# Kernel tuning notes

Measured on AMD Instinct MI355X. Metric: run time of the kernel, lower is better.

The kernel has to match this reference:

```python
import jax, jax.numpy as jnp
import numpy as np

N = 100000       # num_nodes
E = 1600000      # num edges
C = 1000         # num_communities
NE = 128         # n_embedding
NID = 64         # n_id_embedding
NH = 128         # n_hidden


def setup_inputs() -> dict:
    key = jax.random.key(0)
    ks = jax.random.split(key, 24)
    s = 0.05  # small init scale for weights
    inp = {
        "x": jax.random.normal(ks[0], (N, 19), dtype=jnp.float32),
        "edge_index": jax.random.randint(ks[1], (2, E), 0, N, dtype=jnp.int64),
        "community": jax.random.randint(ks[2], (N,), 0, C, dtype=jnp.int64),
        "id_embeddings": jax.random.normal(ks[3], (N, NID), dtype=jnp.float32),
        "W_emb1": jax.random.normal(ks[4], (7, NE), dtype=jnp.float32) * s,
        "b_emb1": jnp.zeros((NE,), jnp.float32),
        "W_emb2": jax.random.normal(ks[5], (12, NE), dtype=jnp.float32) * s,
        "b_emb2": jnp.zeros((NE,), jnp.float32),
        "W_emb3": jax.random.normal(ks[6], (2 * NE + NID, 2 * NE + NID), dtype=jnp.float32) * s,
        "b_emb3": jnp.zeros((2 * NE + NID,), jnp.float32),
        "W_conv1": jax.random.normal(ks[7], (2 * NE + NID, NH), dtype=jnp.float32) * s,
        "b_conv1": jnp.zeros((NH,), jnp.float32),
        "W_conv2": jax.random.normal(ks[8], (NH, NH), dtype=jnp.float32) * s,
        "b_conv2": jnp.zeros((NH,), jnp.float32),
        "W_lin1": jax.random.normal(ks[9], (2 * NH, NH), dtype=jnp.float32) * s,
        "b_lin1": jnp.zeros((NH,), jnp.float32),
        "W_lin2": jax.random.normal(ks[10], (NH, 1), dtype=jnp.float32) * s,
        "b_lin2": jnp.zeros((1,), jnp.float32),
    }
    return inp


def _gcn_conv(h, W, b, src, dst, deg_inv_sqrt):
    # PyG GCNConv: D^{-1/2}(A+I)D^{-1/2} (h W) + b, self-loops included.
    hw = h @ W                                   # [N, out]
    norm = deg_inv_sqrt[src] * deg_inv_sqrt[dst]  # [E]
    msg = hw[src] * norm[:, None]                # [E, out] gather
    agg = jax.ops.segment_sum(msg, dst, num_segments=N)
    agg = agg + hw * (deg_inv_sqrt ** 2)[:, None]  # self-loop term (norm = 1/deg)
    return agg + b


def _community_pool(h, community):
    # scatter_mean over community ids, then cat([mean, mean], dim=1)
    sums = jax.ops.segment_sum(h, community, num_segments=C)
    cnt = jax.ops.segment_sum(jnp.ones((h.shape[0],), h.dtype), community, num_segments=C)
    mean = sums / jnp.maximum(cnt, 1.0)[:, None]
    return jnp.concatenate([mean, mean], axis=1)


def reference(x, edge_index, community, id_embeddings,
              W_emb1, b_emb1, W_emb2, b_emb2, W_emb3, b_emb3,
              W_conv1, b_conv1, W_conv2, b_conv2,
              W_lin1, b_lin1, W_lin2, b_lin2):
    src, dst = edge_index[0], edge_index[1]
    # degree (with self-loops) on dst, as in PyG gcn_norm
    deg = jax.ops.segment_sum(jnp.ones((E,), jnp.float32), dst, num_segments=N) + 1.0
    deg_inv_sqrt = deg ** -0.5

    x1 = jax.nn.relu(x[:, :7] @ W_emb1 + b_emb1)
    x2 = jax.nn.relu(x[:, 7:] @ W_emb2 + b_emb2)
    h = jnp.concatenate([x1, x2, id_embeddings], axis=1)   # [N, 320]
    h = jax.nn.relu(h @ W_emb3 + b_emb3)

    h = jax.nn.relu(_gcn_conv(h, W_conv1, b_conv1, src, dst, deg_inv_sqrt))
    p1 = _community_pool(h, community)                      # [C, 2*NH]
    h = jax.nn.relu(_gcn_conv(h, W_conv2, b_conv2, src, dst, deg_inv_sqrt))
    p2 = _community_pool(h, community)                      # [C, 2*NH]

    z = p1 + p2
    z = jax.nn.relu(z @ W_lin1 + b_lin1)
    # dropout is identity in eval mode (training=False)
    out = (z @ W_lin2 + b_lin2).squeeze(-1)                 # [C]
    return out
```

## Files before the change

### kernel.cpp

```cpp
#include <hip/hip_runtime.h>
#include <hip/hip_bf16.h>
#include <cstddef>

#define NN 100000
#define EE 1600000
#define CC 1000
#define NBK ((NN + 255) / 256)
#define EPB 4096

#define FP8_SCALE 32.0f
#define FP8_INV   0.03125f

using short8 = __attribute__((ext_vector_type(8))) short;
using f32x4  = __attribute__((ext_vector_type(4))) float;
using f32x2  = __attribute__((ext_vector_type(2))) float;

__device__ __forceinline__ float bf2f(unsigned int u) {
    union { unsigned int i; float f; } x; x.i = u << 16; return x.f;
}
__device__ __forceinline__ unsigned short f2bf(float f) {
    __hip_bfloat16 h = __float2bfloat16(f);
    return *reinterpret_cast<unsigned short*>(&h);
}
__device__ __forceinline__ unsigned int pack2(float lo, float hi) {
    return ((unsigned int)f2bf(hi) << 16) | f2bf(lo);
}
__device__ __forceinline__ unsigned char f2fp8(float v) {
    unsigned int p = __builtin_amdgcn_cvt_pk_fp8_f32(v, v, 0, false);
    return (unsigned char)(p & 0xffu);
}
__device__ __forceinline__ f32x2 fp8x2f(unsigned int u16) {
    return __builtin_amdgcn_cvt_pk_f32_fp8(u16, false);
}

__global__ void k_init(int* __restrict__ bucketCnt, int* __restrict__ bucketFill,
                       int* __restrict__ commcnt) {
    int i = blockIdx.x * 256 + threadIdx.x;
    if (i < NBK) { bucketCnt[i] = 0; bucketFill[i] = 0; }
    if (i < CC) commcnt[i] = 0;
}

__global__ __launch_bounds__(256) void k_bhist(const int* __restrict__ dst,
                                               int* __restrict__ bucketCnt) {
    __shared__ int hist[NBK];
    int t = threadIdx.x;
    for (int i = t; i < NBK; i += 256) hist[i] = 0;
    __syncthreads();
    int base = blockIdx.x * EPB;
    for (int i = t; i < EPB; i += 256) {
        int e = base + i;
        if (e < EE) atomicAdd(&hist[dst[e] >> 8], 1);
    }
    __syncthreads();
    for (int i = t; i < NBK; i += 256)
        if (hist[i]) atomicAdd(&bucketCnt[i], hist[i]);
}

__global__ void k_bscan(const int* __restrict__ bucketCnt, int* __restrict__ bucketBase) {
    __shared__ int sd[512];
    int t = threadIdx.x;
    int v = (t < NBK) ? bucketCnt[t] : 0;
    sd[t] = v;
    __syncthreads();
    for (int off = 1; off < 512; off <<= 1) {
        int x = (t >= off) ? sd[t - off] : 0;
        __syncthreads();
        sd[t] += x;
        __syncthreads();
    }
    if (t < NBK) bucketBase[t] = sd[t] - v;
    if (t == 0) bucketBase[NBK] = EE;
}

__global__ __launch_bounds__(256) void k_bucketize(
    const int* __restrict__ src, const int* __restrict__ dst,
    const int* __restrict__ bucketBase, int* __restrict__ bucketFill,
    int2* __restrict__ bkt) {
    __shared__ int hist[NBK];
    __shared__ int runPos[NBK];
    int t = threadIdx.x;
    for (int i = t; i < NBK; i += 256) hist[i] = 0;
    __syncthreads();
    int base = blockIdx.x * EPB;
    for (int i = t; i < EPB; i += 256) {
        int e = base + i;
        if (e < EE) atomicAdd(&hist[dst[e] >> 8], 1);
    }
    __syncthreads();
    for (int i = t; i < NBK; i += 256)
        runPos[i] = hist[i] ? (bucketBase[i] + atomicAdd(&bucketFill[i], hist[i])) : 0;
    __syncthreads();
    for (int i = t; i < EPB; i += 256) {
        int e = base + i;
        if (e < EE) {
            int d = dst[e];
            int pos = atomicAdd(&runPos[d >> 8], 1);
            bkt[pos] = make_int2(src[e], d);
        }
    }
}

__global__ __launch_bounds__(256) void k_csr(
    const int2* __restrict__ bkt, const int* __restrict__ bucketBase,
    const int* __restrict__ comm, int* __restrict__ commcnt,
    int* __restrict__ rowofs, float* __restrict__ dis, int* __restrict__ csr) {
    __shared__ int cnt[256], sd[256], cnt2[256];
    int b = blockIdx.x, t = threadIdx.x;
    int base = bucketBase[b], end = bucketBase[b + 1];
    int nodeBase = b << 8;
    cnt[t] = 0; cnt2[t] = 0;
    __syncthreads();
    for (int i = base + t; i < end; i += 256)
        atomicAdd(&cnt[bkt[i].y - nodeBase], 1);
    __syncthreads();
    int v = cnt[t];
    sd[t] = v;
    __syncthreads();
    for (int off = 1; off < 256; off <<= 1) {
        int x = (t >= off) ? sd[t - off] : 0;
        __syncthreads();
        sd[t] += x;
        __syncthreads();
    }
    int ofs = sd[t] - v;
    sd[t] = ofs;
    int node = nodeBase + t;
    if (node < NN) {
        rowofs[node] = base + ofs;
        dis[node] = rsqrtf((float)v + 1.0f);
        atomicAdd(&commcnt[comm[node]], 1);
    }
    if (b == NBK - 1 && t == 0) rowofs[NN] = EE;
    __syncthreads();
    for (int i = base + t; i < end; i += 256) {
        int2 ed = bkt[i];
        int ld = ed.y - nodeBase;
        int p = atomicAdd(&cnt2[ld], 1);
        csr[base + sd[ld] + p] = ed.x;
    }
}

__global__ void k_scanc(int* __restrict__ commcnt, int* __restrict__ commofs) {
    __shared__ int sd[1024];
    int t = threadIdx.x;
    int v = (t < CC) ? commcnt[t] : 0;
    sd[t] = v;
    __syncthreads();
    for (int off = 1; off < 1024; off <<= 1) {
        int x = (t >= off) ? sd[t - off] : 0;
        __syncthreads();
        sd[t] += x;
        __syncthreads();
    }
    if (t < CC) {
        commofs[t] = sd[t] - v;
        commcnt[t] = 0;
    }
    if (t == CC - 1) commofs[CC] = sd[t];
}

__global__ void k_fillc(const int* __restrict__ comm, const int* __restrict__ commofs,
                        int* __restrict__ commcnt, int* __restrict__ members) {
    int i = blockIdx.x * 256 + threadIdx.x;
    if (i >= NN) return;
    int c = comm[i];
    int pos = commofs[c] + atomicAdd(&commcnt[c], 1);
    members[pos] = i;
}

__global__ void k_wconv(const float* __restrict__ W3, unsigned short* __restrict__ W3t,
                        const float* __restrict__ Wc1, unsigned short* __restrict__ Wc1t,
                        const float* __restrict__ Wc2, unsigned short* __restrict__ Wc2t) {
    int y = blockIdx.y;
    int k = blockIdx.x * 256 + threadIdx.x;
    if (y < 320) {
        if (k < 328) W3t[(size_t)y * 328 + k] = (k < 320) ? f2bf(W3[(size_t)k * 320 + y]) : 0;
    } else if (y < 448) {
        int n = y - 320;
        if (k < 328) Wc1t[(size_t)n * 328 + k] = (k < 320) ? f2bf(Wc1[(size_t)k * 128 + n]) : 0;
    } else {
        int n = y - 448;
        if (k < 136) Wc2t[(size_t)n * 136 + k] = (k < 128) ? f2bf(Wc2[(size_t)k * 128 + n]) : 0;
    }
}

__global__ __launch_bounds__(256) void k_embed(
    const float* __restrict__ x, const float* __restrict__ id_emb,
    const float* __restrict__ W1, const float* __restrict__ b1,
    const float* __restrict__ W2, const float* __restrict__ b2,
    unsigned short* __restrict__ h0) {
    __shared__ float W1s[7][128];
    __shared__ float W2s[12][128];
    __shared__ float b1s[128], b2s[128];
    __shared__ float xs[64][20];
    int t = threadIdx.x;
    int base = blockIdx.x * 64;
    for (int i = t; i < 7 * 128; i += 256) ((float*)W1s)[i] = W1[i];
    for (int i = t; i < 12 * 128; i += 256) ((float*)W2s)[i] = W2[i];
    if (t < 128) { b1s[t] = b1[t]; b2s[t] = b2[t]; }
    for (int i = t; i < 64 * 19; i += 256) {
        int r = i / 19, cc = i % 19;
        int node = base + r;
        xs[r][cc] = (node < NN) ? x[(size_t)node * 19 + cc] : 0.f;
    }
    __syncthreads();
    int ln = t >> 6, lane = t & 63;
    int c2 = lane * 2;
    for (int nn = ln; nn < 64; nn += 4) {
        int node = base + nn;
        if (node >= NN) break;
        unsigned int* orow = (unsigned int*)(h0 + (size_t)node * 320);
        float a0 = b1s[c2], a1 = b1s[c2 + 1];
        #pragma unroll
        for (int k = 0; k < 7; ++k) {
            float xv = xs[nn][k];
            float2 w = *(const float2*)&W1s[k][c2];
            a0 += xv * w.x; a1 += xv * w.y;
        }
        orow[lane] = pack2(fmaxf(a0, 0.f), fmaxf(a1, 0.f));
        a0 = b2s[c2]; a1 = b2s[c2 + 1];
        #pragma unroll
        for (int k = 0; k < 12; ++k) {
            float xv = xs[nn][7 + k];
            float2 w = *(const float2*)&W2s[k][c2];
            a0 += xv * w.x; a1 += xv * w.y;
        }
        orow[64 + lane] = pack2(fmaxf(a0, 0.f), fmaxf(a1, 0.f));
        if (lane < 32) {
            float2 iv = *(const float2*)(id_emb + (size_t)node * 64 + c2);
            orow[128 + lane] = pack2(iv.x, iv.y);
        }
    }
}

template <int K, int N, int RELU, int OUT8>
__global__ __launch_bounds__(256) void k_bgemm(
    const unsigned short* __restrict__ A, const unsigned short* __restrict__ Bt,
    const float* __restrict__ bias, void* __restrict__ Cv, int M) {
    constexpr int NT = (N + 127) / 128;
    __shared__ __align__(16) short sbuf[2][10240];
    int t = threadIdx.x;
    int bid = blockIdx.x;
    if constexpr (NT > 1) {
        int nwg = gridDim.x;
        int q = nwg >> 3, r = nwg & 7;
        int xcd = bid & 7, idx = bid >> 3;
        bid = (xcd < r ? xcd * (q + 1) : r * (q + 1) + (xcd - r) * q) + idx;
    }
    int ct = bid % NT, rblk = bid / NT;
    int rowBase = rblk * 128, colBase = ct * 128;
    int wid = t >> 6, lane = t & 63;
    int wm = wid >> 1, wn = wid & 1;
    int fr = lane & 15, g = lane >> 4;
    int rr = t >> 2;
    int qq = (t & 3) * 8;
    f32x4 acc[4][4] = {};
    short8 z = {};
    short8 pA0, pA1, pB0, pB1;
    int grA0 = rowBase + rr, grA1 = grA0 + 64;
    int gcB0 = colBase + rr, gcB1 = gcB0 + 64;
    pA0 = (grA0 < M) ? *(const short8*)(A + (size_t)grA0 * K + qq) : z;
    pA1 = (grA1 < M) ? *(const short8*)(A + (size_t)grA1 * K + qq) : z;
    pB0 = (gcB0 < N) ? *(const short8*)(Bt + (size_t)gcB0 * (K + 8) + qq) : z;
    pB1 = (gcB1 < N) ? *(const short8*)(Bt + (size_t)gcB1 * (K + 8) + qq) : z;
    {
        short* As = sbuf[0];
        short* Bs = sbuf[0] + 128 * 40;
        *(short8*)&As[rr * 40 + qq]        = pA0;
        *(short8*)&As[(rr + 64) * 40 + qq] = pA1;
        *(short8*)&Bs[rr * 40 + qq]        = pB0;
        *(short8*)&Bs[(rr + 64) * 40 + qq] = pB1;
    }
    __syncthreads();
    int cur = 0;
    for (int kb = 0; kb < K; kb += 32) {
        bool more = (kb + 32 < K);
        if (more) {
            int kn = kb + 32;
            pA0 = (grA0 < M) ? *(const short8*)(A + (size_t)grA0 * K + kn + qq) : z;
            pA1 = (grA1 < M) ? *(const short8*)(A + (size_t)grA1 * K + kn + qq) : z;
            pB0 = (gcB0 < N) ? *(const short8*)(Bt + (size_t)gcB0 * (K + 8) + kn + qq) : z;
            pB1 = (gcB1 < N) ? *(const short8*)(Bt + (size_t)gcB1 * (K + 8) + kn + qq) : z;
        }
        const short* As = sbuf[cur];
        const short* Bs = sbuf[cur] + 128 * 40;
        short8 bfr[4];
        #pragma unroll
        for (int nf = 0; nf < 4; ++nf)
            bfr[nf] = *(const short8*)&Bs[(wn * 64 + nf * 16 + fr) * 40 + g * 8];
        #pragma unroll
        for (int mf = 0; mf < 4; ++mf) {
            short8 a = *(const short8*)&As[(wm * 64 + mf * 16 + fr) * 40 + g * 8];
            #pragma unroll
            for (int nf = 0; nf < 4; ++nf)
                acc[mf][nf] = __builtin_amdgcn_mfma_f32_16x16x32_bf16(a, bfr[nf], acc[mf][nf], 0, 0, 0);
        }
        if (more) {
            short* Asn = sbuf[cur ^ 1];
            short* Bsn = sbuf[cur ^ 1] + 128 * 40;
            *(short8*)&Asn[rr * 40 + qq]        = pA0;
            *(short8*)&Asn[(rr + 64) * 40 + qq] = pA1;
            *(short8*)&Bsn[rr * 40 + qq]        = pB0;
            *(short8*)&Bsn[(rr + 64) * 40 + qq] = pB1;
        }
        __syncthreads();
        cur ^= 1;
    }
    if (!OUT8) {
        unsigned short* sb = (unsigned short*)sbuf[0];
        #pragma unroll
        for (int cc = 0; cc < 2; ++cc) {
            int cbase = colBase + cc * 64;
            if (cbase < N) {
                if (cc) __syncthreads();
                if (wn == cc) {
                    #pragma unroll
                    for (int nf = 0; nf < 4; ++nf) {
                        int colL = nf * 16 + fr;
                        float bv = RELU ? bias[cbase + colL] : 0.f;
                        #pragma unroll
                        for (int mf = 0; mf < 4; ++mf) {
                            #pragma unroll
                            for (int r = 0; r < 4; ++r) {
                                int row = wm * 64 + mf * 16 + g * 4 + r;
                                float v = acc[mf][nf][r];
                                if (RELU) v = fmaxf(v + bv, 0.f);
                                sb[row * 72 + colL] = f2bf(v);
                            }
                        }
                    }
                }
                __syncthreads();
                #pragma unroll
                for (int i = 0; i < 4; ++i) {
                    int off8 = t + 256 * i;
                    int row = off8 >> 3;
                    int col = (off8 & 7) * 8;
                    int grow = rowBase + row;
                    if (grow < M)
                        *(short8*)((unsigned short*)Cv + (size_t)grow * N + cbase + col) =
                            *(const short8*)&sb[row * 72 + col];
                }
            }
        }
    } else {
        unsigned char* sb8 = (unsigned char*)sbuf[0];
        #pragma unroll
        for (int nf = 0; nf < 4; ++nf) {
            int colL = wn * 64 + nf * 16 + fr;
            #pragma unroll
            for (int mf = 0; mf < 4; ++mf) {
                #pragma unroll
                for (int r = 0; r < 4; ++r) {
                    int row = wm * 64 + mf * 16 + g * 4 + r;
                    sb8[row * 128 + colL] = f2fp8(acc[mf][nf][r] * FP8_SCALE);
                }
            }
        }
        __syncthreads();
        #pragma unroll
        for (int i = 0; i < 4; ++i) {
            int off16 = t + 256 * i;
            int row = off16 >> 3;
            int col = (off16 & 7) * 16;
            int grow = rowBase + row;
            if (grow < M)
                *(int4*)((unsigned char*)Cv + (size_t)grow * N + col) =
                    *(const int4*)&sb8[row * 128 + col];
        }
    }
}

__global__ __launch_bounds__(256) void k_gather(
    const int* __restrict__ rowofs, const int* __restrict__ csr,
    const float* __restrict__ dis, const unsigned char* __restrict__ hw8,
    const float* __restrict__ bias, unsigned short* __restrict__ hout) {
    int wid = blockIdx.x * 4 + (threadIdx.x >> 6);
    wid = __builtin_amdgcn_readfirstlane(wid);
    int lane = threadIdx.x & 63;
    if (wid >= NN) return;
    int ro = rowofs[wid], re = rowofs[wid + 1];
    int c = lane * 2;
    float dsd = dis[wid];
    unsigned int hv = *(const unsigned short*)(hw8 + (size_t)wid * 128 + c);
    f32x2 hf = fp8x2f(hv);
    float a0 = hf.x * dsd;
    float a1 = hf.y * dsd;
    int e = ro;
    for (; e + 16 <= re; e += 16) {
        int s[16]; float n[16]; unsigned int v[16];
        #pragma unroll
        for (int j = 0; j < 16; ++j) s[j] = csr[e + j];
        #pragma unroll
        for (int j = 0; j < 16; ++j) n[j] = dis[s[j]];
        #pragma unroll
        for (int j = 0; j < 16; ++j)
            v[j] = *(const unsigned short*)(hw8 + (size_t)s[j] * 128 + c);
        #pragma unroll
        for (int j = 0; j < 16; ++j) {
            f32x2 f = fp8x2f(v[j]);
            a0 += f.x * n[j];
            a1 += f.y * n[j];
        }
    }
    for (; e + 4 <= re; e += 4) {
        int s[4]; float n[4]; unsigned int v[4];
        #pragma unroll
        for (int j = 0; j < 4; ++j) s[j] = csr[e + j];
        #pragma unroll
        for (int j = 0; j < 4; ++j) n[j] = dis[s[j]];
        #pragma unroll
        for (int j = 0; j < 4; ++j)
            v[j] = *(const unsigned short*)(hw8 + (size_t)s[j] * 128 + c);
        #pragma unroll
        for (int j = 0; j < 4; ++j) {
            f32x2 f = fp8x2f(v[j]);
            a0 += f.x * n[j];
            a1 += f.y * n[j];
        }
    }
    for (; e < re; ++e) {
        int s0 = csr[e];
        float n0 = dis[s0];
        unsigned int v0 = *(const unsigned short*)(hw8 + (size_t)s0 * 128 + c);
        f32x2 f = fp8x2f(v0);
        a0 += f.x * n0;
        a1 += f.y * n0;
    }
    a0 = fmaxf(a0 * dsd * FP8_INV + bias[c], 0.f);
    a1 = fmaxf(a1 * dsd * FP8_INV + bias[c + 1], 0.f);
    *(unsigned int*)(hout + (size_t)wid * 128 + c) = pack2(a0, a1);
}

__global__ __launch_bounds__(128) void k_final(
    const unsigned short* __restrict__ h2, const unsigned short* __restrict__ h3,
    const int* __restrict__ commofs, const int* __restrict__ members,
    const float* __restrict__ Wl1, const float* __restrict__ bl1,
    const float* __restrict__ Wl2, const float* __restrict__ bl2,
    float* __restrict__ out) {
    __shared__ float zh[128];
    __shared__ float partial[2];
    int c = blockIdx.x, t = threadIdx.x;
    int ro = commofs[c], re = commofs[c + 1];
    float acc = 0.f;
    int e = ro;
    for (; e + 4 <= re; e += 4) {
        int m0 = members[e], m1 = members[e + 1];
        int m2 = members[e + 2], m3 = members[e + 3];
        acc += bf2f(h2[(size_t)m0 * 128 + t]) + bf2f(h3[(size_t)m0 * 128 + t]);
        acc += bf2f(h2[(size_t)m1 * 128 + t]) + bf2f(h3[(size_t)m1 * 128 + t]);
        acc += bf2f(h2[(size_t)m2 * 128 + t]) + bf2f(h3[(size_t)m2 * 128 + t]);
        acc += bf2f(h2[(size_t)m3 * 128 + t]) + bf2f(h3[(size_t)m3 * 128 + t]);
    }
    for (; e < re; ++e) {
        int m = members[e];
        acc += bf2f(h2[(size_t)m * 128 + t]) + bf2f(h3[(size_t)m * 128 + t]);
    }
    float invc = 1.0f / fmaxf((float)(re - ro), 1.0f);
    zh[t] = acc * invc;
    __syncthreads();
    float a = bl1[t];
    for (int k = 0; k < 128; ++k)
        a += zh[k] * (Wl1[(size_t)k * 128 + t] + Wl1[(size_t)(k + 128) * 128 + t]);
    float zv = fmaxf(a, 0.f);
    float p = zv * Wl2[t];
    #pragma unroll
    for (int off = 32; off > 0; off >>= 1) p += __shfl_down(p, off, 64);
    if ((t & 63) == 0) partial[t >> 6] = p;
    __syncthreads();
    if (t == 0) out[c] = partial[0] + partial[1] + bl2[0];
}

extern "C" void kernel_launch(void* const* d_in, const int* in_sizes, int n_in,
                              void* d_out, int out_size, void* d_ws, size_t ws_size,
                              hipStream_t stream) {
    const float* x       = (const float*)d_in[0];
    const int*   edge    = (const int*)d_in[1];
    const int*   comm    = (const int*)d_in[2];
    const float* id_emb  = (const float*)d_in[3];
    const float* W1      = (const float*)d_in[4];
    const float* b1      = (const float*)d_in[5];
    const float* W2      = (const float*)d_in[6];
    const float* b2      = (const float*)d_in[7];
    const float* W3      = (const float*)d_in[8];
    const float* b3      = (const float*)d_in[9];
    const float* Wc1     = (const float*)d_in[10];
    const float* bc1     = (const float*)d_in[11];
    const float* Wc2     = (const float*)d_in[12];
    const float* bc2     = (const float*)d_in[13];
    const float* Wl1     = (const float*)d_in[14];
    const float* bl1     = (const float*)d_in[15];
    const float* Wl2     = (const float*)d_in[16];
    const float* bl2     = (const float*)d_in[17];
    float* out = (float*)d_out;
    float* ws  = (float*)d_ws;

    const int* srcIdx = edge;
    const int* dstIdx = edge + EE;

    size_t o = 0;
    auto alloc = [&](size_t nfloats) {
        float* p = ws + o; o += (nfloats + 3) & ~(size_t)3; return p;
    };
    float* dis      = alloc(NN);
    int* rowofs     = (int*)alloc(NN + 8);
    int* bucketCnt  = (int*)alloc(NBK + 8);
    int* bucketBase = (int*)alloc(NBK + 8);
    int* bucketFill = (int*)alloc(NBK + 8);
    int* commcnt    = (int*)alloc(1024);
    int* commofs    = (int*)alloc(1024 + 8);
    int* members    = (int*)alloc(NN);
    int2* bkt       = (int2*)alloc((size_t)EE * 2);
    int* csr        = (int*)alloc(EE);
    unsigned short* W3t  = (unsigned short*)alloc(320 * 328 / 2);
    unsigned short* Wc1t = (unsigned short*)alloc(128 * 328 / 2);
    unsigned short* Wc2t = (unsigned short*)alloc(128 * 136 / 2);
    unsigned short* h0   = (unsigned short*)alloc((size_t)NN * 320 / 2);
    unsigned short* h1   = (unsigned short*)alloc((size_t)NN * 320 / 2);
    unsigned char*  hw8  = (unsigned char*)alloc((size_t)NN * 128 / 4);
    unsigned short* h2   = (unsigned short*)alloc((size_t)NN * 128 / 2);
    unsigned short* h3   = (unsigned short*)alloc((size_t)NN * 128 / 2);

    k_init<<<4, 256, 0, stream>>>(bucketCnt, bucketFill, commcnt);
    k_bhist<<<NBK, 256, 0, stream>>>(dstIdx, bucketCnt);
    k_bscan<<<1, 512, 0, stream>>>(bucketCnt, bucketBase);
    k_bucketize<<<NBK, 256, 0, stream>>>(srcIdx, dstIdx, bucketBase, bucketFill, bkt);
    k_csr<<<NBK, 256, 0, stream>>>(bkt, bucketBase, comm, commcnt, rowofs, dis, csr);
    k_scanc<<<1, 1024, 0, stream>>>(commcnt, commofs);
    k_fillc<<<NBK, 256, 0, stream>>>(comm, commofs, commcnt, members);

    k_wconv<<<dim3(2, 576), 256, 0, stream>>>(W3, W3t, Wc1, Wc1t, Wc2, Wc2t);

    k_embed<<<(NN + 63) / 64, 256, 0, stream>>>(x, id_emb, W1, b1, W2, b2, h0);

    int rb = (NN + 127) / 128;
    k_bgemm<320, 320, 1, 0><<<rb * 3, 256, 0, stream>>>(h0, W3t, b3, h1, NN);
    k_bgemm<320, 128, 0, 1><<<rb, 256, 0, stream>>>(h1, Wc1t, nullptr, hw8, NN);
    k_gather<<<(NN + 3) / 4, 256, 0, stream>>>(rowofs, csr, dis, hw8, bc1, h2);
    k_bgemm<128, 128, 0, 1><<<rb, 256, 0, stream>>>(h2, Wc2t, nullptr, hw8, NN);
    k_gather<<<(NN + 3) / 4, 256, 0, stream>>>(rowofs, csr, dis, hw8, bc2, h3);

    k_final<<<CC, 128, 0, stream>>>(h2, h3, commofs, members, Wl1, bl1, Wl2, bl2, out);
}
```

Measured before the change: 380.8 us.

## Fuse embedding GEMM and conv1 GEMM into one kernel keeping intermediate in LDS

A new kernel computes relu(h0·W3+b3) for a 64-row tile, keeps the result in shared memory, and immediately multiplies it by Wc1 to produce the FP8 hw8 output. This drops the global write and reread of the 320-wide bf16 intermediate and one kernel launch. The unused bf16 output path and the XCD block remapping are removed from the generic GEMM. The trade-off is large LDS use, which lowers occupancy, plus single-buffered weight tiles reloaded per block with no prefetch overlap.

```diff
diff --git a/kernel.cpp b/kernel.cpp
--- a/kernel.cpp
+++ b/kernel.cpp
@@ -233,6 +233,104 @@
     }
 }
 
+__global__ __launch_bounds__(256) void k_fuse(
+    const unsigned short* __restrict__ h0, const unsigned short* __restrict__ W3t,
+    const float* __restrict__ b3, const unsigned short* __restrict__ Wc1t,
+    unsigned char* __restrict__ hw8, int M) {
+    __shared__ __align__(16) short h0s[64][328];
+    __shared__ __align__(16) short Bs[320][40];
+    int t = threadIdx.x;
+    int rowBase = blockIdx.x * 64;
+    int w = t >> 6, lane = t & 63;
+    int fr = lane & 15, g = lane >> 4;
+    for (int c = t; c < 64 * 40; c += 256) {
+        int r = c / 40, part = c % 40;
+        int grow = rowBase + r;
+        short8 v = {};
+        if (grow < M) v = *(const short8*)(h0 + (size_t)grow * 320 + part * 8);
+        *(short8*)&h0s[r][part * 8] = v;
+    }
+    f32x4 acc1[4][5] = {};
+    for (int kb = 0; kb < 320; kb += 32) {
+        __syncthreads();
+        for (int c = t; c < 320 * 4; c += 256) {
+            int r = c >> 2, q = c & 3;
+            *(short8*)&Bs[r][q * 8] = *(const short8*)(W3t + (size_t)r * 328 + kb + q * 8);
+        }
+        __syncthreads();
+        short8 a[4], b[5];
+        #pragma unroll
+        for (int rf = 0; rf < 4; ++rf)
+            a[rf] = *(const short8*)&h0s[rf * 16 + fr][kb + g * 8];
+        #pragma unroll
+        for (int cf = 0; cf < 5; ++cf)
+            b[cf] = *(const short8*)&Bs[w * 80 + cf * 16 + fr][g * 8];
+        #pragma unroll
+        for (int rf = 0; rf < 4; ++rf)
+            #pragma unroll
+            for (int cf = 0; cf < 5; ++cf)
+                acc1[rf][cf] = __builtin_amdgcn_mfma_f32_16x16x32_bf16(a[rf], b[cf], acc1[rf][cf], 0, 0, 0);
+    }
+    __syncthreads();
+    #pragma unroll
+    for (int cf = 0; cf < 5; ++cf) {
+        int col = w * 80 + cf * 16 + fr;
+        float bv = b3[col];
+        #pragma unroll
+        for (int rf = 0; rf < 4; ++rf) {
+            #pragma unroll
+            for (int r = 0; r < 4; ++r) {
+                int row = rf * 16 + g * 4 + r;
+                h0s[row][col] = (short)f2bf(fmaxf(acc1[rf][cf][r] + bv, 0.f));
+            }
+        }
+    }
+    f32x4 acc2[4][2] = {};
+    for (int kb = 0; kb < 320; kb += 32) {
+        __syncthreads();
+        for (int c = t; c < 128 * 4; c += 256) {
+            int r = c >> 2, q = c & 3;
+            *(short8*)&Bs[r][q * 8] = *(const short8*)(Wc1t + (size_t)r * 328 + kb + q * 8);
+        }
+        __syncthreads();
+        short8 a[4], b[2];
+        #pragma unroll
+        for (int rf = 0; rf < 4; ++rf)
+            a[rf] = *(const short8*)&h0s[rf * 16 + fr][kb + g * 8];
+        #pragma unroll
+        for (int cf = 0; cf < 2; ++cf)
+            b[cf] = *(const short8*)&Bs[w * 32 + cf * 16 + fr][g * 8];
+        #pragma unroll
+        for (int rf = 0; rf < 4; ++rf)
+            #pragma unroll
+            for (int cf = 0; cf < 2; ++cf)
+                acc2[rf][cf] = __builtin_amdgcn_mfma_f32_16x16x32_bf16(a[rf], b[cf], acc2[rf][cf], 0, 0, 0);
+    }
+    unsigned char* sb8 = (unsigned char*)Bs;
+    __syncthreads();
+    #pragma unroll
+    for (int cf = 0; cf < 2; ++cf) {
+        int colL = w * 32 + cf * 16 + fr;
+        #pragma unroll
+        for (int rf = 0; rf < 4; ++rf) {
+            #pragma unroll
+            for (int r = 0; r < 4; ++r) {
+                int row = rf * 16 + g * 4 + r;
+                sb8[row * 128 + colL] = f2fp8(acc2[rf][cf][r] * FP8_SCALE);
+            }
+        }
+    }
+    __syncthreads();
+    #pragma unroll
+    for (int i = 0; i < 2; ++i) {
+        int c16 = t + 256 * i;
+        int row = c16 >> 3, col = (c16 & 7) * 16;
+        int grow = rowBase + row;
+        if (grow < M)
+            *(int4*)(hw8 + (size_t)grow * 128 + col) = *(const int4*)&sb8[row * 128 + col];
+    }
+}
+
 template <int K, int N, int RELU, int OUT8>
 __global__ __launch_bounds__(256) void k_bgemm(
     const unsigned short* __restrict__ A, const unsigned short* __restrict__ Bt,
@@ -241,12 +339,6 @@
     __shared__ __align__(16) short sbuf[2][10240];
     int t = threadIdx.x;
     int bid = blockIdx.x;
-    if constexpr (NT > 1) {
-        int nwg = gridDim.x;
-        int q = nwg >> 3, r = nwg & 7;
-        int xcd = bid & 7, idx = bid >> 3;
-        bid = (xcd < r ? xcd * (q + 1) : r * (q + 1) + (xcd - r) * q) + idx;
-    }
     int ct = bid % NT, rblk = bid / NT;
     int rowBase = rblk * 128, colBase = ct * 128;
     int wid = t >> 6, lane = t & 63;
@@ -306,68 +398,29 @@
         __syncthreads();
         cur ^= 1;
     }
-    if (!OUT8) {
-        unsigned short* sb = (unsigned short*)sbuf[0];
-        #pragma unroll
-        for (int cc = 0; cc < 2; ++cc) {
-            int cbase = colBase + cc * 64;
-            if (cbase < N) {
-                if (cc) __syncthreads();
-                if (wn == cc) {
-                    #pragma unroll
-                    for (int nf = 0; nf < 4; ++nf) {
-                        int colL = nf * 16 + fr;
-                        float bv = RELU ? bias[cbase + colL] : 0.f;
-                        #pragma unroll
-                        for (int mf = 0; mf < 4; ++mf) {
-                            #pragma unroll
-                            for (int r = 0; r < 4; ++r) {
-                                int row = wm * 64 + mf * 16 + g * 4 + r;
-                                float v = acc[mf][nf][r];
-                                if (RELU) v = fmaxf(v + bv, 0.f);
-                                sb[row * 72 + colL] = f2bf(v);
-                            }
-                        }
-                    }
-                }
-                __syncthreads();
-                #pragma unroll
-                for (int i = 0; i < 4; ++i) {
-                    int off8 = t + 256 * i;
-                    int row = off8 >> 3;
-                    int col = (off8 & 7) * 8;
-                    int grow = rowBase + row;
-                    if (grow < M)
-                        *(short8*)((unsigned short*)Cv + (size_t)grow * N + cbase + col) =
-                            *(const short8*)&sb[row * 72 + col];
-                }
+    unsigned char* sb8 = (unsigned char*)sbuf[0];
+    #pragma unroll
+    for (int nf = 0; nf < 4; ++nf) {
+        int colL = wn * 64 + nf * 16 + fr;
+        #pragma unroll
+        for (int mf = 0; mf < 4; ++mf) {
+            #pragma unroll
+            for (int r = 0; r < 4; ++r) {
+                int row = wm * 64 + mf * 16 + g * 4 + r;
+                sb8[row * 128 + colL] = f2fp8(acc[mf][nf][r] * FP8_SCALE);
             }
         }
-    } else {
-        unsigned char* sb8 = (unsigned char*)sbuf[0];
-        #pragma unroll
-        for (int nf = 0; nf < 4; ++nf) {
-            int colL = wn * 64 + nf * 16 + fr;
-            #pragma unroll
-            for (int mf = 0; mf < 4; ++mf) {
-                #pragma unroll
-                for (int r = 0; r < 4; ++r) {
-                    int row = wm * 64 + mf * 16 + g * 4 + r;
-                    sb8[row * 128 + colL] = f2fp8(acc[mf][nf][r] * FP8_SCALE);
-                }
-            }
-        }
-        __syncthreads();
-        #pragma unroll
-        for (int i = 0; i < 4; ++i) {
-            int off16 = t + 256 * i;
-            int row = off16 >> 3;
-            int col = (off16 & 7) * 16;
-            int grow = rowBase + row;
-            if (grow < M)
-                *(int4*)((unsigned char*)Cv + (size_t)grow * N + col) =
-                    *(const int4*)&sb8[row * 128 + col];
-        }
+    }
+    __syncthreads();
+    #pragma unroll
+    for (int i = 0; i < 4; ++i) {
+        int off16 = t + 256 * i;
+        int row = off16 >> 3;
+        int col = (off16 & 7) * 16;
+        int grow = rowBase + row;
+        if (grow < M)
+            *(int4*)((unsigned char*)Cv + (size_t)grow * N + col) =
+                *(const int4*)&sb8[row * 128 + col];
     }
 }
 
@@ -516,7 +569,6 @@
     unsigned short* Wc1t = (unsigned short*)alloc(128 * 328 / 2);
     unsigned short* Wc2t = (unsigned short*)alloc(128 * 136 / 2);
     unsigned short* h0   = (unsigned short*)alloc((size_t)NN * 320 / 2);
-    unsigned short* h1   = (unsigned short*)alloc((size_t)NN * 320 / 2);
     unsigned char*  hw8  = (unsigned char*)alloc((size_t)NN * 128 / 4);
     unsigned short* h2   = (unsigned short*)alloc((size_t)NN * 128 / 2);
     unsigned short* h3   = (unsigned short*)alloc((size_t)NN * 128 / 2);
@@ -533,11 +585,9 @@
 
     k_embed<<<(NN + 63) / 64, 256, 0, stream>>>(x, id_emb, W1, b1, W2, b2, h0);
 
-    int rb = (NN + 127) / 128;
-    k_bgemm<320, 320, 1, 0><<<rb * 3, 256, 0, stream>>>(h0, W3t, b3, h1, NN);
-    k_bgemm<320, 128, 0, 1><<<rb, 256, 0, stream>>>(h1, Wc1t, nullptr, hw8, NN);
+    k_fuse<<<(NN + 63) / 64, 256, 0, stream>>>(h0, W3t, b3, Wc1t, hw8, NN);
     k_gather<<<(NN + 3) / 4, 256, 0, stream>>>(rowofs, csr, dis, hw8, bc1, h2);
-    k_bgemm<128, 128, 0, 1><<<rb, 256, 0, stream>>>(h2, Wc2t, nullptr, hw8, NN);
+    k_bgemm<128, 128, 0, 1><<<(NN + 127) / 128, 256, 0, stream>>>(h2, Wc2t, nullptr, hw8, NN);
     k_gather<<<(NN + 3) / 4, 256, 0, stream>>>(rowofs, csr, dis, hw8, bc2, h3);
 
     k_final<<<CC, 128, 0, stream>>>(h2, h3, commofs, members, Wl1, bl1, Wl2, bl2, out);
```

Result: slower. 397.3 us (+4.3%).
